# Kernel optimization log

Hardware: AMD Instinct MI355X
Metric: run time of the kernel (lower is better)

The kernel has to match this reference:

```python
import jax, jax.numpy as jnp
import numpy as np

N = 100000      # nodes
E = 1600000     # edges (avg degree 16)
D_IN, HID, D_OUT = 128, 64, 64


def setup_inputs() -> dict:
    key = jax.random.key(0)
    ks = jax.random.split(key, 32)
    rn = lambda k, shape, s=0.1: jax.random.normal(k, shape, jnp.float32) * s
    inp = {
        "x": jax.random.normal(ks[0], (N, D_IN), jnp.float32),
        "edge_index": jax.random.randint(ks[1], (2, E), 0, N, dtype=jnp.int32),
        # GAT layer 1: in=128, heads=2, C=64, concat -> 128
        "w1": rn(ks[2], (D_IN, 2 * HID)), "as1": rn(ks[3], (2, HID)),
        "ad1": rn(ks[4], (2, HID)), "b1": rn(ks[5], (2 * HID,)),
        # GAT layer 2: in=128, heads=2, C=64, concat -> 128
        "w2": rn(ks[6], (2 * HID, 2 * HID)), "as2": rn(ks[7], (2, HID)),
        "ad2": rn(ks[8], (2, HID)), "b2": rn(ks[9], (2 * HID,)),
        # GAT layer 3: in=128, heads=1, C=64, mean -> 64
        "w3": rn(ks[10], (2 * HID, D_OUT)), "as3": rn(ks[11], (1, D_OUT)),
        "ad3": rn(ks[12], (1, D_OUT)), "b3": rn(ks[13], (D_OUT,)),
        # BatchNorm (eval mode: running stats)
        "g1": 1.0 + rn(ks[14], (2 * HID,)), "be1": rn(ks[15], (2 * HID,)),
        "m1": rn(ks[16], (2 * HID,), 0.01), "v1": 1.0 + 0.1 * jax.random.uniform(ks[17], (2 * HID,)),
        "g2": 1.0 + rn(ks[18], (2 * HID,)), "be2": rn(ks[19], (2 * HID,)),
        "m2": rn(ks[20], (2 * HID,), 0.01), "v2": 1.0 + 0.1 * jax.random.uniform(ks[21], (2 * HID,)),
        "g3": 1.0 + rn(ks[22], (D_OUT,)), "be3": rn(ks[23], (D_OUT,)),
        "m3": rn(ks[24], (D_OUT,), 0.01), "v3": 1.0 + 0.1 * jax.random.uniform(ks[25], (D_OUT,)),
    }
    return inp


def _gat(h, W, a_s, a_d, b, src, dst, n, heads, concat):
    """PyG GATConv (eval, add_self_loops already applied to src/dst)."""
    C = a_s.shape[1]
    xl = (h @ W).reshape(n, heads, C)                      # [N,H,C]
    es = jnp.sum(xl * a_s, axis=-1)                        # [N,H] att_src . x
    ed = jnp.sum(xl * a_d, axis=-1)                        # [N,H]
    e = jax.nn.leaky_relu(es[src] + ed[dst], 0.2)          # [E',H]
    mx = jax.ops.segment_max(e, dst, num_segments=n)       # segment softmax over dst
    ex = jnp.exp(e - mx[dst])
    den = jax.ops.segment_sum(ex, dst, num_segments=n)
    alpha = ex / (den[dst] + 1e-16)                        # [E',H]
    out = jax.ops.segment_sum(xl[src] * alpha[:, :, None], dst, num_segments=n)
    out = out.reshape(n, heads * C) if concat else out.mean(axis=1)
    return out + b


def _bn(z, g, be, m, v):
    return (z - m) * jax.lax.rsqrt(v + 1e-5) * g + be


def reference(x, edge_index, w1, as1, ad1, b1, w2, as2, ad2, b2, w3, as3, ad3, b3,
              g1, be1, m1, v1, g2, be2, m2, v2, g3, be3, m3, v3):
    n = x.shape[0]
    loop = jnp.arange(n, dtype=edge_index.dtype)
    src = jnp.concatenate([edge_index[0], loop])           # GATConv add_self_loops=True
    dst = jnp.concatenate([edge_index[1], loop])
    z = jax.nn.relu(_bn(_gat(x, w1, as1, ad1, b1, src, dst, n, 2, True), g1, be1, m1, v1))
    z = jax.nn.relu(_bn(_gat(z, w2, as2, ad2, b2, src, dst, n, 2, True), g2, be2, m2, v2))
    z = _bn(_gat(z, w3, as3, ad3, b3, src, dst, n, 1, False), g3, be3, m3, v3)
    return z
```

## Files before the change

### kernel.cpp

```cpp
#include <hip/hip_runtime.h>
#include <hip/hip_bf16.h>
#include <cstdint>
#include <cstddef>

#define NBLK 512
#define BSH 8

typedef short bf16x8 __attribute__((ext_vector_type(8)));
typedef float f32x4 __attribute__((ext_vector_type(4)));

__device__ __forceinline__ float leaky02(float x) { return x > 0.f ? x : 0.2f * x; }
__device__ __forceinline__ float bflo(unsigned u) { return __uint_as_float(u << 16); }
__device__ __forceinline__ float bfhi(unsigned u) { return __uint_as_float(u & 0xFFFF0000u); }
__device__ __forceinline__ unsigned short f2bf(float f) {
  __hip_bfloat16 h = __float2bfloat16(f);
  return *(unsigned short*)&h;
}
__device__ __forceinline__ unsigned pack2bf(float a, float b) {
  return (unsigned)f2bf(a) | ((unsigned)f2bf(b) << 16);
}

__global__ void bucket_hist(const int* __restrict__ dst, int* __restrict__ T,
                            int E, int N, int NB, int echunk, int nchunk,
                            const float* __restrict__ w1, const float* __restrict__ w2,
                            const float* __restrict__ w3,
                            unsigned short* __restrict__ t1, unsigned short* __restrict__ t2,
                            unsigned short* __restrict__ t3) {
  int b = blockIdx.x, t = threadIdx.x;
  if (b >= NBLK) {
    int bb = b - NBLK;
    const float* W; unsigned short* Tw; int NO; int e;
    if (bb < 64)      { W = w1; Tw = t1; NO = 128; e = bb * 256 + t; }
    else if (bb < 128){ W = w2; Tw = t2; NO = 128; e = (bb - 64) * 256 + t; }
    else              { W = w3; Tw = t3; NO = 64;  e = (bb - 128) * 256 + t; }
    int c = e >> 7, k = e & 127;
    Tw[c * 128 + k] = f2bf(W[k * NO + c]);
    return;
  }
  __shared__ int hist[512];
  hist[t] = 0; hist[t + 256] = 0;
  __syncthreads();
  int e0 = b * echunk, e1 = min(E, e0 + echunk);
  for (int e = e0 + t; e < e1; e += 256) atomicAdd(&hist[dst[e] >> BSH], 1);
  int n0 = b * nchunk, n1 = min(N, n0 + nchunk);
  for (int nn = n0 + t; nn < n1; nn += 256) atomicAdd(&hist[nn >> BSH], 1);
  __syncthreads();
  for (int k = t; k < NB; k += 256) if (hist[k]) atomicAdd(&T[k], hist[k]);
}

__global__ void scan_small(const int* __restrict__ T, int* __restrict__ B,
                           int* __restrict__ C, int NB) {
  __shared__ int wsum[8];
  int t = threadIdx.x;
  int val = (t < NB) ? T[t] : 0;
  int lane = t & 63, wid = t >> 6;
  int incl = val;
  for (int off = 1; off < 64; off <<= 1) {
    int o = __shfl_up(incl, off);
    if (lane >= off) incl += o;
  }
  if (lane == 63) wsum[wid] = incl;
  __syncthreads();
  if (t == 0) { int r = 0; for (int i = 0; i < 8; ++i) { int x = wsum[i]; wsum[i] = r; r += x; } }
  __syncthreads();
  int excl = incl - val + wsum[wid];
  if (t <= NB) B[t] = excl;
  if (t < NB) C[t] = excl;
}

__global__ void bucketB2(const int* __restrict__ src, const int* __restrict__ dst,
                         int* __restrict__ C, unsigned* __restrict__ binned,
                         int E, int N, int NB, int echunk, int nchunk) {
  __shared__ int hist[512];
  __shared__ int cur[512];
  int b = blockIdx.x, t = threadIdx.x;
  hist[t] = 0; hist[t + 256] = 0;
  __syncthreads();
  int e0 = b * echunk, e1 = min(E, e0 + echunk);
  for (int e = e0 + t; e < e1; e += 256) atomicAdd(&hist[dst[e] >> BSH], 1);
  int n0 = b * nchunk, n1 = min(N, n0 + nchunk);
  for (int nn = n0 + t; nn < n1; nn += 256) atomicAdd(&hist[nn >> BSH], 1);
  __syncthreads();
  for (int k = t; k < 512; k += 256) {
    int c = hist[k];
    cur[k] = c ? atomicAdd(&C[k], c) : 0;
  }
  __syncthreads();
  for (int e = e0 + t; e < e1; e += 256) {
    int d = dst[e];
    int k = d >> BSH;
    int pos = atomicAdd(&cur[k], 1);
    binned[pos] = (unsigned)src[e] | ((unsigned)(d & 255) << 24);
  }
  for (int nn = n0 + t; nn < n1; nn += 256) {
    int k = nn >> BSH;
    int pos = atomicAdd(&cur[k], 1);
    binned[pos] = (unsigned)nn | ((unsigned)(nn & 255) << 24);
  }
}

__global__ void bucketC2(const unsigned* __restrict__ binned, const int* __restrict__ B,
                         int* __restrict__ rowp, int* __restrict__ col, int N) {
  __shared__ int cnt2[256];
  __shared__ int cur2[256];
  __shared__ int wsum[4];
  int k = blockIdx.x, t = threadIdx.x;
  int base = B[k];
  int end  = B[k + 1];
  cnt2[t] = 0;
  __syncthreads();
  for (int e = base + t; e < end; e += 256) atomicAdd(&cnt2[binned[e] >> 24], 1);
  __syncthreads();
  int v = cnt2[t];
  int incl = v;
  int lane = t & 63, wid = t >> 6;
  for (int off = 1; off < 64; off <<= 1) {
    int o = __shfl_up(incl, off);
    if (lane >= off) incl += o;
  }
  if (lane == 63) wsum[wid] = incl;
  __syncthreads();
  if (t == 0) { int r = 0; for (int i = 0; i < 4; ++i) { int x2 = wsum[i]; wsum[i] = r; r += x2; } }
  __syncthreads();
  int excl = incl - v + wsum[wid];
  int g = (k << BSH) + t;
  if (g <= N) rowp[g] = base + excl;
  cur2[t] = excl;
  __syncthreads();
  for (int e = base + t; e < end; e += 256) {
    unsigned p = binned[e];
    int pos = atomicAdd(&cur2[p >> 24], 1);
    col[base + pos] = (int)(p & 0xFFFFFFu);
  }
}

template<int NO, bool F32IN>
__launch_bounds__(256)
__global__ void gemm_mfma(const void* __restrict__ Xp,
                          const unsigned short* __restrict__ Wt,
                          unsigned short* __restrict__ Y, int n,
                          const float* __restrict__ as, const float* __restrict__ ad,
                          float* __restrict__ es, float* __restrict__ ed) {
  constexpr int NT = NO / 16;
  const int wid = threadIdx.x >> 6, lane = threadIdx.x & 63;
  const int wr0 = (blockIdx.x * 4 + wid) * 32;
  if (wr0 >= n) return;
  const int cl = lane & 15, kg = lane >> 4;

  int r0c = wr0 + cl;      if (r0c > n - 1) r0c = n - 1;
  int r1c = wr0 + 16 + cl; if (r1c > n - 1) r1c = n - 1;

  f32x4 acc[2][NT] = {};
  const unsigned short* Xb = (const unsigned short*)Xp;
  const float* Xf = (const float*)Xp;

#pragma unroll
  for (int ks = 0; ks < 4; ++ks) {
    bf16x8 a0, a1;
    if constexpr (F32IN) {
      const float* p0 = Xf + (size_t)r0c * 128 + kg * 8 + ks * 32;
      const float* p1 = Xf + (size_t)r1c * 128 + kg * 8 + ks * 32;
      float4 u0 = *(const float4*)p0, u1 = *(const float4*)(p0 + 4);
      float4 w0 = *(const float4*)p1, w1 = *(const float4*)(p1 + 4);
      a0[0] = (short)f2bf(u0.x); a0[1] = (short)f2bf(u0.y); a0[2] = (short)f2bf(u0.z); a0[3] = (short)f2bf(u0.w);
      a0[4] = (short)f2bf(u1.x); a0[5] = (short)f2bf(u1.y); a0[6] = (short)f2bf(u1.z); a0[7] = (short)f2bf(u1.w);
      a1[0] = (short)f2bf(w0.x); a1[1] = (short)f2bf(w0.y); a1[2] = (short)f2bf(w0.z); a1[3] = (short)f2bf(w0.w);
      a1[4] = (short)f2bf(w1.x); a1[5] = (short)f2bf(w1.y); a1[6] = (short)f2bf(w1.z); a1[7] = (short)f2bf(w1.w);
    } else {
      a0 = *(const bf16x8*)(Xb + (size_t)r0c * 128 + kg * 8 + ks * 32);
      a1 = *(const bf16x8*)(Xb + (size_t)r1c * 128 + kg * 8 + ks * 32);
    }
#pragma unroll
    for (int t = 0; t < NT; ++t) {
      bf16x8 bb = *(const bf16x8*)(Wt + (size_t)(cl + t * 16) * 128 + kg * 8 + ks * 32);
      acc[0][t] = __builtin_amdgcn_mfma_f32_16x16x32_bf16(a0, bb, acc[0][t], 0, 0, 0);
      acc[1][t] = __builtin_amdgcn_mfma_f32_16x16x32_bf16(a1, bb, acc[1][t], 0, 0, 0);
    }
  }

  float asv[NT], adv[NT];
#pragma unroll
  for (int t = 0; t < NT; ++t) { asv[t] = as[t * 16 + cl]; adv[t] = ad[t * 16 + cl]; }

#pragma unroll
  for (int s = 0; s < 2; ++s) {
#pragma unroll
    for (int rg = 0; rg < 4; ++rg) {
      int r = wr0 + s * 16 + kg * 4 + rg;
      float ps0 = 0.f, pd0 = 0.f, ps1 = 0.f, pd1 = 0.f;
#pragma unroll
      for (int t = 0; t < NT; ++t) {
        float a = acc[s][t][rg];
        if (NO == 128 && t >= 4) { ps1 = fmaf(a, asv[t], ps1); pd1 = fmaf(a, adv[t], pd1); }
        else                     { ps0 = fmaf(a, asv[t], ps0); pd0 = fmaf(a, adv[t], pd0); }
      }
#pragma unroll
      for (int o = 8; o; o >>= 1) {
        ps0 += __shfl_xor(ps0, o); pd0 += __shfl_xor(pd0, o);
        if (NO == 128) { ps1 += __shfl_xor(ps1, o); pd1 += __shfl_xor(pd1, o); }
      }
      if (r < n) {
        if (cl == 0) {
          if (NO == 128) {
            es[(size_t)r * 2] = ps0; es[(size_t)r * 2 + 1] = ps1;
            ed[(size_t)r * 2] = pd0; ed[(size_t)r * 2 + 1] = pd1;
          } else {
            es[r] = ps0; ed[r] = pd0;
          }
        }
#pragma unroll
        for (int t = 0; t < NT; ++t)
          Y[(size_t)r * NO + t * 16 + cl] = f2bf(acc[s][t][rg]);
      }
    }
  }
}

__launch_bounds__(256)
__global__ void aggregate2(const unsigned short* __restrict__ xl, const float* __restrict__ es,
                           const float* __restrict__ ed, const int* __restrict__ rowp,
                           const int* __restrict__ col, const float* __restrict__ bias,
                           const float* __restrict__ g, const float* __restrict__ be,
                           const float* __restrict__ m, const float* __restrict__ v,
                           uint4* __restrict__ out, int n) {
  int node = (blockIdx.x * blockDim.x + threadIdx.x) >> 6;
  int lane = threadIdx.x & 63;
  if (node >= n) return;
  const uint4* xr = (const uint4*)xl;
  int beg = rowp[node], end = rowp[node + 1];
  float2 edv = *(const float2*)&ed[(size_t)node * 2];
  const int q = lane >> 4, hl = lane & 15;

  float acc[8] = {0.f, 0.f, 0.f, 0.f, 0.f, 0.f, 0.f, 0.f};
  float dl0 = 0.f, dl1 = 0.f;

  for (int cb = beg; cb < end; cb += 64) {
    int idx = cb + lane;
    int s = 0; float w0 = 0.f, w1 = 0.f;
    if (idx < end) {
      s = col[idx];
      float2 e2 = *(const float2*)&es[(size_t)s * 2];
      w0 = __expf(leaky02(e2.x + edv.x));
      w1 = __expf(leaky02(e2.y + edv.y));
    }
    dl0 += w0; dl1 += w1;
    int cend = end - cb; if (cend > 64) cend = 64;
    int i = 0;
    for (; i + 8 <= cend; i += 8) {
      int j0 = i + q, j1 = i + 4 + q;
      int s0 = __shfl(s, j0), s1 = __shfl(s, j1);
      uint4 v0 = xr[(size_t)s0 * 16 + hl];
      uint4 v1 = xr[(size_t)s1 * 16 + hl];
      float w00 = __shfl(w0, j0), w01 = __shfl(w1, j0);
      float w10 = __shfl(w0, j1), w11 = __shfl(w1, j1);
      float W0 = (hl < 8) ? w00 : w01;
      float W1 = (hl < 8) ? w10 : w11;
      acc[0] = fmaf(W0, bflo(v0.x), acc[0]); acc[1] = fmaf(W0, bfhi(v0.x), acc[1]);
      acc[2] = fmaf(W0, bflo(v0.y), acc[2]); acc[3] = fmaf(W0, bfhi(v0.y), acc[3]);
      acc[4] = fmaf(W0, bflo(v0.z), acc[4]); acc[5] = fmaf(W0, bfhi(v0.z), acc[5]);
      acc[6] = fmaf(W0, bflo(v0.w), acc[6]); acc[7] = fmaf(W0, bfhi(v0.w), acc[7]);
      acc[0] = fmaf(W1, bflo(v1.x), acc[0]); acc[1] = fmaf(W1, bfhi(v1.x), acc[1]);
      acc[2] = fmaf(W1, bflo(v1.y), acc[2]); acc[3] = fmaf(W1, bfhi(v1.y), acc[3]);
      acc[4] = fmaf(W1, bflo(v1.z), acc[4]); acc[5] = fmaf(W1, bfhi(v1.z), acc[5]);
      acc[6] = fmaf(W1, bflo(v1.w), acc[6]); acc[7] = fmaf(W1, bfhi(v1.w), acc[7]);
    }
    for (; i < cend; i += 4) {
      int j = i + q;
      int s0 = __shfl(s, j);
      uint4 v0 = xr[(size_t)s0 * 16 + hl];
      float w00 = __shfl(w0, j), w01 = __shfl(w1, j);
      float W0 = (hl < 8) ? w00 : w01;
      acc[0] = fmaf(W0, bflo(v0.x), acc[0]); acc[1] = fmaf(W0, bfhi(v0.x), acc[1]);
      acc[2] = fmaf(W0, bflo(v0.y), acc[2]); acc[3] = fmaf(W0, bfhi(v0.y), acc[3]);
      acc[4] = fmaf(W0, bflo(v0.z), acc[4]); acc[5] = fmaf(W0, bfhi(v0.z), acc[5]);
      acc[6] = fmaf(W0, bflo(v0.w), acc[6]); acc[7] = fmaf(W0, bfhi(v0.w), acc[7]);
    }
  }

#pragma unroll
  for (int k2 = 0; k2 < 8; ++k2) {
    acc[k2] += __shfl_xor(acc[k2], 16);
    acc[k2] += __shfl_xor(acc[k2], 32);
  }
#pragma unroll
  for (int o = 32; o; o >>= 1) { dl0 += __shfl_xor(dl0, o); dl1 += __shfl_xor(dl1, o); }

  if (q == 0) {
    int c0 = hl * 8;
    float den = (hl < 8) ? dl0 : dl1;
    float inv = 1.f / (den + 1e-16f);
    float4 bi0 = *(const float4*)&bias[c0], bi1 = *(const float4*)&bias[c0 + 4];
    float4 mm0 = *(const float4*)&m[c0],    mm1 = *(const float4*)&m[c0 + 4];
    float4 vv0 = *(const float4*)&v[c0],    vv1 = *(const float4*)&v[c0 + 4];
    float4 gg0 = *(const float4*)&g[c0],    gg1 = *(const float4*)&g[c0 + 4];
    float4 bb0 = *(const float4*)&be[c0],   bb1 = *(const float4*)&be[c0 + 4];
    float r0 = (acc[0] * inv + bi0.x - mm0.x) * rsqrtf(vv0.x + 1e-5f) * gg0.x + bb0.x;
    float r1 = (acc[1] * inv + bi0.y - mm0.y) * rsqrtf(vv0.y + 1e-5f) * gg0.y + bb0.y;
    float r2 = (acc[2] * inv + bi0.z - mm0.z) * rsqrtf(vv0.z + 1e-5f) * gg0.z + bb0.z;
    float r3 = (acc[3] * inv + bi0.w - mm0.w) * rsqrtf(vv0.w + 1e-5f) * gg0.w + bb0.w;
    float r4 = (acc[4] * inv + bi1.x - mm1.x) * rsqrtf(vv1.x + 1e-5f) * gg1.x + bb1.x;
    float r5 = (acc[5] * inv + bi1.y - mm1.y) * rsqrtf(vv1.y + 1e-5f) * gg1.y + bb1.y;
    float r6 = (acc[6] * inv + bi1.z - mm1.z) * rsqrtf(vv1.z + 1e-5f) * gg1.z + bb1.z;
    float r7 = (acc[7] * inv + bi1.w - mm1.w) * rsqrtf(vv1.w + 1e-5f) * gg1.w + bb1.w;
    uint4 o;
    o.x = pack2bf(fmaxf(r0, 0.f), fmaxf(r1, 0.f));
    o.y = pack2bf(fmaxf(r2, 0.f), fmaxf(r3, 0.f));
    o.z = pack2bf(fmaxf(r4, 0.f), fmaxf(r5, 0.f));
    o.w = pack2bf(fmaxf(r6, 0.f), fmaxf(r7, 0.f));
    out[(size_t)node * 16 + hl] = o;
  }
}

__launch_bounds__(256)
__global__ void aggregate1(const unsigned short* __restrict__ xl, const float* __restrict__ es,
                           const float* __restrict__ ed, const int* __restrict__ rowp,
                           const int* __restrict__ col, const float* __restrict__ bias,
                           const float* __restrict__ g, const float* __restrict__ be,
                           const float* __restrict__ m, const float* __restrict__ v,
                           float* __restrict__ out, int n) {
  int node = (blockIdx.x * blockDim.x + threadIdx.x) >> 6;
  int lane = threadIdx.x & 63;
  if (node >= n) return;
  const uint4* xr = (const uint4*)xl;
  int beg = rowp[node], end = rowp[node + 1];
  float edv = ed[node];
  const int g8 = lane >> 3, hl = lane & 7;

  float acc[8] = {0.f, 0.f, 0.f, 0.f, 0.f, 0.f, 0.f, 0.f};
  float dl = 0.f;

  for (int cb = beg; cb < end; cb += 64) {
    int idx = cb + lane;
    int s = 0; float w = 0.f;
    if (idx < end) {
      s = col[idx];
      w = __expf(leaky02(es[s] + edv));
    }
    dl += w;
    int cend = end - cb; if (cend > 64) cend = 64;
    int i = 0;
    for (; i + 16 <= cend; i += 16) {
      int j0 = i + g8, j1 = i + 8 + g8;
      int s0 = __shfl(s, j0), s1 = __shfl(s, j1);
      uint4 v0 = xr[(size_t)s0 * 8 + hl];
      uint4 v1 = xr[(size_t)s1 * 8 + hl];
      float W0 = __shfl(w, j0), W1 = __shfl(w, j1);
      acc[0] = fmaf(W0, bflo(v0.x), acc[0]); acc[1] = fmaf(W0, bfhi(v0.x), acc[1]);
      acc[2] = fmaf(W0, bflo(v0.y), acc[2]); acc[3] = fmaf(W0, bfhi(v0.y), acc[3]);
      acc[4] = fmaf(W0, bflo(v0.z), acc[4]); acc[5] = fmaf(W0, bfhi(v0.z), acc[5]);
      acc[6] = fmaf(W0, bflo(v0.w), acc[6]); acc[7] = fmaf(W0, bfhi(v0.w), acc[7]);
      acc[0] = fmaf(W1, bflo(v1.x), acc[0]); acc[1] = fmaf(W1, bfhi(v1.x), acc[1]);
      acc[2] = fmaf(W1, bflo(v1.y), acc[2]); acc[3] = fmaf(W1, bfhi(v1.y), acc[3]);
      acc[4] = fmaf(W1, bflo(v1.z), acc[4]); acc[5] = fmaf(W1, bfhi(v1.z), acc[5]);
      acc[6] = fmaf(W1, bflo(v1.w), acc[6]); acc[7] = fmaf(W1, bfhi(v1.w), acc[7]);
    }
    for (; i < cend; i += 8) {
      int j = i + g8;
      int s0 = __shfl(s, j);
      uint4 v0 = xr[(size_t)s0 * 8 + hl];
      float W0 = __shfl(w, j);
      acc[0] = fmaf(W0, bflo(v0.x), acc[0]); acc[1] = fmaf(W0, bfhi(v0.x), acc[1]);
      acc[2] = fmaf(W0, bflo(v0.y), acc[2]); acc[3] = fmaf(W0, bfhi(v0.y), acc[3]);
      acc[4] = fmaf(W0, bflo(v0.z), acc[4]); acc[5] = fmaf(W0, bfhi(v0.z), acc[5]);
      acc[6] = fmaf(W0, bflo(v0.w), acc[6]); acc[7] = fmaf(W0, bfhi(v0.w), acc[7]);
    }
  }

#pragma unroll
  for (int k2 = 0; k2 < 8; ++k2) {
    acc[k2] += __shfl_xor(acc[k2], 8);
    acc[k2] += __shfl_xor(acc[k2], 16);
    acc[k2] += __shfl_xor(acc[k2], 32);
  }
#pragma unroll
  for (int o = 32; o; o >>= 1) dl += __shfl_xor(dl, o);

  if (lane < 8) {
    int c0 = hl * 8;
    float inv = 1.f / (dl + 1e-16f);
    float4 bi0 = *(const float4*)&bias[c0], bi1 = *(const float4*)&bias[c0 + 4];
    float4 mm0 = *(const float4*)&m[c0],    mm1 = *(const float4*)&m[c0 + 4];
    float4 vv0 = *(const float4*)&v[c0],    vv1 = *(const float4*)&v[c0 + 4];
    float4 gg0 = *(const float4*)&g[c0],    gg1 = *(const float4*)&g[c0 + 4];
    float4 bb0 = *(const float4*)&be[c0],   bb1 = *(const float4*)&be[c0 + 4];
    float4 ra, rb;
    ra.x = (acc[0] * inv + bi0.x - mm0.x) * rsqrtf(vv0.x + 1e-5f) * gg0.x + bb0.x;
    ra.y = (acc[1] * inv + bi0.y - mm0.y) * rsqrtf(vv0.y + 1e-5f) * gg0.y + bb0.y;
    ra.z = (acc[2] * inv + bi0.z - mm0.z) * rsqrtf(vv0.z + 1e-5f) * gg0.z + bb0.z;
    ra.w = (acc[3] * inv + bi0.w - mm0.w) * rsqrtf(vv0.w + 1e-5f) * gg0.w + bb0.w;
    rb.x = (acc[4] * inv + bi1.x - mm1.x) * rsqrtf(vv1.x + 1e-5f) * gg1.x + bb1.x;
    rb.y = (acc[5] * inv + bi1.y - mm1.y) * rsqrtf(vv1.y + 1e-5f) * gg1.y + bb1.y;
    rb.z = (acc[6] * inv + bi1.z - mm1.z) * rsqrtf(vv1.z + 1e-5f) * gg1.z + bb1.z;
    rb.w = (acc[7] * inv + bi1.w - mm1.w) * rsqrtf(vv1.w + 1e-5f) * gg1.w + bb1.w;
    float4* op = (float4*)(out + (size_t)node * 64 + c0);
    op[0] = ra; op[1] = rb;
  }
}

extern "C" void kernel_launch(void* const* d_in, const int* in_sizes, int n_in,
                              void* d_out, int out_size, void* d_ws, size_t ws_size,
                              hipStream_t stream) {
  const float* x   = (const float*)d_in[0];
  const int*   ei  = (const int*)d_in[1];
  const float* w1  = (const float*)d_in[2];
  const float* as1 = (const float*)d_in[3];
  const float* ad1 = (const float*)d_in[4];
  const float* b1  = (const float*)d_in[5];
  const float* w2  = (const float*)d_in[6];
  const float* as2 = (const float*)d_in[7];
  const float* ad2 = (const float*)d_in[8];
  const float* b2  = (const float*)d_in[9];
  const float* w3  = (const float*)d_in[10];
  const float* as3 = (const float*)d_in[11];
  const float* ad3 = (const float*)d_in[12];
  const float* b3  = (const float*)d_in[13];
  const float* g1  = (const float*)d_in[14];
  const float* be1 = (const float*)d_in[15];
  const float* m1  = (const float*)d_in[16];
  const float* v1  = (const float*)d_in[17];
  const float* g2  = (const float*)d_in[18];
  const float* be2 = (const float*)d_in[19];
  const float* m2  = (const float*)d_in[20];
  const float* v2  = (const float*)d_in[21];
  const float* g3  = (const float*)d_in[22];
  const float* be3 = (const float*)d_in[23];
  const float* m3  = (const float*)d_in[24];
  const float* v3  = (const float*)d_in[25];

  const int N = in_sizes[0] / 128;
  const int E = in_sizes[1] / 2;
  const int Etot = E + N;
  const int* srcp = ei;
  const int* dstp = ei + E;
  const int NB = (N + 255) >> BSH;
  const int echunk = (E + NBLK - 1) / NBLK;
  const int nchunk = (N + NBLK - 1) / NBLK;

  size_t off = 0;
  auto carve = [&](size_t bytes) {
    void* p = (char*)d_ws + off;
    off += (bytes + 255) & ~(size_t)255;
    return p;
  };
  unsigned short* Xb  = (unsigned short*)carve((size_t)N * 128 * 2);
  unsigned short* Yb  = (unsigned short*)carve((size_t)N * 128 * 2);
  float* esb  = (float*)carve((size_t)N * 2 * 4);
  float* edb  = (float*)carve((size_t)N * 2 * 4);
  int*   rowp = (int*)carve((size_t)(N + 1) * 4);
  int*   col  = (int*)carve((size_t)Etot * 4);
  unsigned* binned = (unsigned*)carve((size_t)Etot * 4);
  int* T = (int*)carve(512 * 4);
  int* B = (int*)carve(513 * 4);
  int* C = (int*)carve(512 * 4);
  unsigned short* Wt1 = (unsigned short*)carve(128 * 128 * 2);
  unsigned short* Wt2 = (unsigned short*)carve(128 * 128 * 2);
  unsigned short* Wt3 = (unsigned short*)carve(128 * 64 * 2);
  (void)ws_size; (void)n_in; (void)out_size;

  hipMemsetAsync(T, 0, NB * 4, stream);
  bucket_hist<<<NBLK + 160, 256, 0, stream>>>(dstp, T, E, N, NB, echunk, nchunk,
                                              w1, w2, w3, Wt1, Wt2, Wt3);
  scan_small<<<1, 512, 0, stream>>>(T, B, C, NB);
  bucketB2<<<NBLK, 256, 0, stream>>>(srcp, dstp, C, binned, E, N, NB, echunk, nchunk);
  bucketC2<<<NB, 256, 0, stream>>>(binned, B, rowp, col, N);

  const int gemm_grid = (N + 127) / 128;
  const int agg_grid  = (N + 3) / 4;

  gemm_mfma<128, true><<<gemm_grid, 256, 0, stream>>>(x, Wt1, Yb, N, as1, ad1, esb, edb);
  aggregate2<<<agg_grid, 256, 0, stream>>>(Yb, esb, edb, rowp, col, b1, g1, be1, m1, v1,
                                           (uint4*)Xb, N);
  gemm_mfma<128, false><<<gemm_grid, 256, 0, stream>>>(Xb, Wt2, Yb, N, as2, ad2, esb, edb);
  aggregate2<<<agg_grid, 256, 0, stream>>>(Yb, esb, edb, rowp, col, b2, g2, be2, m2, v2,
                                           (uint4*)Xb, N);
  gemm_mfma<64, false><<<gemm_grid, 256, 0, stream>>>(Xb, Wt3, Yb, N, as3, ad3, esb, edb);
  aggregate1<<<agg_grid, 256, 0, stream>>>(Yb, esb, edb, rowp, col, b3, g3, be3, m3, v3,
                                           (float*)d_out, N);
}
```

Measured before the change: 348.3 us.

## Use fixed-capacity buckets and fuse CSR sort with first GEMM

Replaces the histogram/scan/bin/sort pipeline with fixed-capacity per-bucket regions so no global prefix scan is needed, cutting the CSR build to two kernels. The per-bucket local sort runs in the same launch as the layer-1 GEMM so the two overlap, and sorts in place from an LDS copy. Aggregation kernels now read separate row begin/end arrays. The cost is a larger workspace, and any bucket exceeding the fixed capacity would be truncated.

```diff
diff --git a/kernel.cpp b/kernel.cpp
--- a/kernel.cpp
+++ b/kernel.cpp
@@ -5,6 +5,8 @@
 
 #define NBLK 512
 #define BSH 8
+#define CAPSH 13
+#define CAP (1 << CAPSH)
 
 typedef short bf16x8 __attribute__((ext_vector_type(8)));
 typedef float f32x4 __attribute__((ext_vector_type(4)));
@@ -20,130 +22,15 @@
   return (unsigned)f2bf(a) | ((unsigned)f2bf(b) << 16);
 }
 
-__global__ void bucket_hist(const int* __restrict__ dst, int* __restrict__ T,
-                            int E, int N, int NB, int echunk, int nchunk,
-                            const float* __restrict__ w1, const float* __restrict__ w2,
-                            const float* __restrict__ w3,
-                            unsigned short* __restrict__ t1, unsigned short* __restrict__ t2,
-                            unsigned short* __restrict__ t3) {
-  int b = blockIdx.x, t = threadIdx.x;
-  if (b >= NBLK) {
-    int bb = b - NBLK;
-    const float* W; unsigned short* Tw; int NO; int e;
-    if (bb < 64)      { W = w1; Tw = t1; NO = 128; e = bb * 256 + t; }
-    else if (bb < 128){ W = w2; Tw = t2; NO = 128; e = (bb - 64) * 256 + t; }
-    else              { W = w3; Tw = t3; NO = 64;  e = (bb - 128) * 256 + t; }
-    int c = e >> 7, k = e & 127;
-    Tw[c * 128 + k] = f2bf(W[k * NO + c]);
-    return;
-  }
-  __shared__ int hist[512];
-  hist[t] = 0; hist[t + 256] = 0;
-  __syncthreads();
-  int e0 = b * echunk, e1 = min(E, e0 + echunk);
-  for (int e = e0 + t; e < e1; e += 256) atomicAdd(&hist[dst[e] >> BSH], 1);
-  int n0 = b * nchunk, n1 = min(N, n0 + nchunk);
-  for (int nn = n0 + t; nn < n1; nn += 256) atomicAdd(&hist[nn >> BSH], 1);
-  __syncthreads();
-  for (int k = t; k < NB; k += 256) if (hist[k]) atomicAdd(&T[k], hist[k]);
-}
-
-__global__ void scan_small(const int* __restrict__ T, int* __restrict__ B,
-                           int* __restrict__ C, int NB) {
-  __shared__ int wsum[8];
-  int t = threadIdx.x;
-  int val = (t < NB) ? T[t] : 0;
-  int lane = t & 63, wid = t >> 6;
-  int incl = val;
-  for (int off = 1; off < 64; off <<= 1) {
-    int o = __shfl_up(incl, off);
-    if (lane >= off) incl += o;
-  }
-  if (lane == 63) wsum[wid] = incl;
-  __syncthreads();
-  if (t == 0) { int r = 0; for (int i = 0; i < 8; ++i) { int x = wsum[i]; wsum[i] = r; r += x; } }
-  __syncthreads();
-  int excl = incl - val + wsum[wid];
-  if (t <= NB) B[t] = excl;
-  if (t < NB) C[t] = excl;
-}
-
-__global__ void bucketB2(const int* __restrict__ src, const int* __restrict__ dst,
-                         int* __restrict__ C, unsigned* __restrict__ binned,
-                         int E, int N, int NB, int echunk, int nchunk) {
-  __shared__ int hist[512];
-  __shared__ int cur[512];
-  int b = blockIdx.x, t = threadIdx.x;
-  hist[t] = 0; hist[t + 256] = 0;
-  __syncthreads();
-  int e0 = b * echunk, e1 = min(E, e0 + echunk);
-  for (int e = e0 + t; e < e1; e += 256) atomicAdd(&hist[dst[e] >> BSH], 1);
-  int n0 = b * nchunk, n1 = min(N, n0 + nchunk);
-  for (int nn = n0 + t; nn < n1; nn += 256) atomicAdd(&hist[nn >> BSH], 1);
-  __syncthreads();
-  for (int k = t; k < 512; k += 256) {
-    int c = hist[k];
-    cur[k] = c ? atomicAdd(&C[k], c) : 0;
-  }
-  __syncthreads();
-  for (int e = e0 + t; e < e1; e += 256) {
-    int d = dst[e];
-    int k = d >> BSH;
-    int pos = atomicAdd(&cur[k], 1);
-    binned[pos] = (unsigned)src[e] | ((unsigned)(d & 255) << 24);
-  }
-  for (int nn = n0 + t; nn < n1; nn += 256) {
-    int k = nn >> BSH;
-    int pos = atomicAdd(&cur[k], 1);
-    binned[pos] = (unsigned)nn | ((unsigned)(nn & 255) << 24);
-  }
-}
-
-__global__ void bucketC2(const unsigned* __restrict__ binned, const int* __restrict__ B,
-                         int* __restrict__ rowp, int* __restrict__ col, int N) {
-  __shared__ int cnt2[256];
-  __shared__ int cur2[256];
-  __shared__ int wsum[4];
-  int k = blockIdx.x, t = threadIdx.x;
-  int base = B[k];
-  int end  = B[k + 1];
-  cnt2[t] = 0;
-  __syncthreads();
-  for (int e = base + t; e < end; e += 256) atomicAdd(&cnt2[binned[e] >> 24], 1);
-  __syncthreads();
-  int v = cnt2[t];
-  int incl = v;
-  int lane = t & 63, wid = t >> 6;
-  for (int off = 1; off < 64; off <<= 1) {
-    int o = __shfl_up(incl, off);
-    if (lane >= off) incl += o;
-  }
-  if (lane == 63) wsum[wid] = incl;
-  __syncthreads();
-  if (t == 0) { int r = 0; for (int i = 0; i < 4; ++i) { int x2 = wsum[i]; wsum[i] = r; r += x2; } }
-  __syncthreads();
-  int excl = incl - v + wsum[wid];
-  int g = (k << BSH) + t;
-  if (g <= N) rowp[g] = base + excl;
-  cur2[t] = excl;
-  __syncthreads();
-  for (int e = base + t; e < end; e += 256) {
-    unsigned p = binned[e];
-    int pos = atomicAdd(&cur2[p >> 24], 1);
-    col[base + pos] = (int)(p & 0xFFFFFFu);
-  }
-}
-
 template<int NO, bool F32IN>
-__launch_bounds__(256)
-__global__ void gemm_mfma(const void* __restrict__ Xp,
+__device__ void gemm_body(int bx, const void* __restrict__ Xp,
                           const unsigned short* __restrict__ Wt,
                           unsigned short* __restrict__ Y, int n,
                           const float* __restrict__ as, const float* __restrict__ ad,
                           float* __restrict__ es, float* __restrict__ ed) {
   constexpr int NT = NO / 16;
   const int wid = threadIdx.x >> 6, lane = threadIdx.x & 63;
-  const int wr0 = (blockIdx.x * 4 + wid) * 32;
+  const int wr0 = (bx * 4 + wid) * 32;
   if (wr0 >= n) return;
   const int cl = lane & 15, kg = lane >> 4;
 
@@ -217,8 +104,115 @@
 }
 
 __launch_bounds__(256)
+__global__ void mega1(const int* __restrict__ src, const int* __restrict__ dst,
+                      int* __restrict__ T, unsigned* __restrict__ binned,
+                      int E, int N, int NB, int echunk, int nchunk,
+                      const float* __restrict__ w1, const float* __restrict__ w2,
+                      const float* __restrict__ w3,
+                      unsigned short* __restrict__ t1, unsigned short* __restrict__ t2,
+                      unsigned short* __restrict__ t3) {
+  int b = blockIdx.x, t = threadIdx.x;
+  if (b >= NBLK) {
+    int bb = b - NBLK;
+    const float* W; unsigned short* Tw; int NO; int e;
+    if (bb < 64)      { W = w1; Tw = t1; NO = 128; e = bb * 256 + t; }
+    else if (bb < 128){ W = w2; Tw = t2; NO = 128; e = (bb - 64) * 256 + t; }
+    else              { W = w3; Tw = t3; NO = 64;  e = (bb - 128) * 256 + t; }
+    int c = e >> 7, k = e & 127;
+    Tw[c * 128 + k] = f2bf(W[k * NO + c]);
+    return;
+  }
+  __shared__ int hist[512];
+  __shared__ int cur[512];
+  hist[t] = 0; hist[t + 256] = 0;
+  __syncthreads();
+  int e0 = b * echunk, e1 = min(E, e0 + echunk);
+  for (int e = e0 + t; e < e1; e += 256) atomicAdd(&hist[dst[e] >> BSH], 1);
+  int n0 = b * nchunk, n1 = min(N, n0 + nchunk);
+  for (int nn = n0 + t; nn < n1; nn += 256) atomicAdd(&hist[nn >> BSH], 1);
+  __syncthreads();
+  for (int k = t; k < 512; k += 256) {
+    int c = hist[k];
+    cur[k] = c ? (k << CAPSH) + atomicAdd(&T[k], c) : 0;
+  }
+  __syncthreads();
+  for (int e = e0 + t; e < e1; e += 256) {
+    int d = dst[e];
+    int k = d >> BSH;
+    int pos = atomicAdd(&cur[k], 1);
+    binned[pos] = (unsigned)src[e] | ((unsigned)(d & 255) << 24);
+  }
+  for (int nn = n0 + t; nn < n1; nn += 256) {
+    int k = nn >> BSH;
+    int pos = atomicAdd(&cur[k], 1);
+    binned[pos] = (unsigned)nn | ((unsigned)(nn & 255) << 24);
+  }
+}
+
+__launch_bounds__(256)
+__global__ void mega2(unsigned* __restrict__ binned, const int* __restrict__ T,
+                      int* __restrict__ rowp, int* __restrict__ rowe, int N, int NB,
+                      const float* __restrict__ x, const unsigned short* __restrict__ Wt1,
+                      unsigned short* __restrict__ Y,
+                      const float* __restrict__ as1, const float* __restrict__ ad1,
+                      float* __restrict__ es, float* __restrict__ ed) {
+  int b = blockIdx.x, t = threadIdx.x;
+  if (b >= NB) {
+    gemm_body<128, true>(b - NB, x, Wt1, Y, N, as1, ad1, es, ed);
+    return;
+  }
+  __shared__ unsigned pay[CAP];
+  __shared__ int cnt2[256];
+  __shared__ int cur2[256];
+  __shared__ int wsum[4];
+  int k = b;
+  int base = k << CAPSH;
+  int cnt = T[k]; if (cnt > CAP) cnt = CAP;
+  cnt2[t] = 0;
+  __syncthreads();
+  for (int e = t; e < cnt; e += 256) {
+    unsigned p = binned[base + e];
+    pay[e] = p;
+    atomicAdd(&cnt2[p >> 24], 1);
+  }
+  __syncthreads();
+  int v = cnt2[t];
+  int incl = v;
+  int lane = t & 63, wid = t >> 6;
+  for (int off = 1; off < 64; off <<= 1) {
+    int o = __shfl_up(incl, off);
+    if (lane >= off) incl += o;
+  }
+  if (lane == 63) wsum[wid] = incl;
+  __syncthreads();
+  if (t == 0) { int r = 0; for (int i = 0; i < 4; ++i) { int x2 = wsum[i]; wsum[i] = r; r += x2; } }
+  __syncthreads();
+  int excl = incl - v + wsum[wid];
+  int g = (k << BSH) + t;
+  if (g < N) { rowp[g] = base + excl; rowe[g] = base + excl + v; }
+  cur2[t] = excl;
+  __syncthreads();
+  for (int e = t; e < cnt; e += 256) {
+    unsigned p = pay[e];
+    int pos = atomicAdd(&cur2[p >> 24], 1);
+    binned[base + pos] = p & 0xFFFFFFu;
+  }
+}
+
+template<int NO, bool F32IN>
+__launch_bounds__(256)
+__global__ void gemm_mfma(const void* __restrict__ Xp,
+                          const unsigned short* __restrict__ Wt,
+                          unsigned short* __restrict__ Y, int n,
+                          const float* __restrict__ as, const float* __restrict__ ad,
+                          float* __restrict__ es, float* __restrict__ ed) {
+  gemm_body<NO, F32IN>(blockIdx.x, Xp, Wt, Y, n, as, ad, es, ed);
+}
+
+__launch_bounds__(256)
 __global__ void aggregate2(const unsigned short* __restrict__ xl, const float* __restrict__ es,
                            const float* __restrict__ ed, const int* __restrict__ rowp,
+                           const int* __restrict__ rowe,
                            const int* __restrict__ col, const float* __restrict__ bias,
                            const float* __restrict__ g, const float* __restrict__ be,
                            const float* __restrict__ m, const float* __restrict__ v,
@@ -227,7 +221,7 @@
   int lane = threadIdx.x & 63;
   if (node >= n) return;
   const uint4* xr = (const uint4*)xl;
-  int beg = rowp[node], end = rowp[node + 1];
+  int beg = rowp[node], end = rowe[node];
   float2 edv = *(const float2*)&ed[(size_t)node * 2];
   const int q = lane >> 4, hl = lane & 15;
 
@@ -314,6 +308,7 @@
 __launch_bounds__(256)
 __global__ void aggregate1(const unsigned short* __restrict__ xl, const float* __restrict__ es,
                            const float* __restrict__ ed, const int* __restrict__ rowp,
+                           const int* __restrict__ rowe,
                            const int* __restrict__ col, const float* __restrict__ bias,
                            const float* __restrict__ g, const float* __restrict__ be,
                            const float* __restrict__ m, const float* __restrict__ v,
@@ -322,7 +317,7 @@
   int lane = threadIdx.x & 63;
   if (node >= n) return;
   const uint4* xr = (const uint4*)xl;
-  int beg = rowp[node], end = rowp[node + 1];
+  int beg = rowp[node], end = rowe[node];
   float edv = ed[node];
   const int g8 = lane >> 3, hl = lane & 7;
 
@@ -429,7 +424,6 @@
 
   const int N = in_sizes[0] / 128;
   const int E = in_sizes[1] / 2;
-  const int Etot = E + N;
   const int* srcp = ei;
   const int* dstp = ei + E;
   const int NB = (N + 255) >> BSH;
@@ -446,34 +440,31 @@
   unsigned short* Yb  = (unsigned short*)carve((size_t)N * 128 * 2);
   float* esb  = (float*)carve((size_t)N * 2 * 4);
   float* edb  = (float*)carve((size_t)N * 2 * 4);
-  int*   rowp = (int*)carve((size_t)(N + 1) * 4);
-  int*   col  = (int*)carve((size_t)Etot * 4);
-  unsigned* binned = (unsigned*)carve((size_t)Etot * 4);
+  int*   rowp = (int*)carve((size_t)N * 4);
+  int*   rowe = (int*)carve((size_t)N * 4);
+  unsigned* binned = (unsigned*)carve((size_t)NB * CAP * 4);
   int* T = (int*)carve(512 * 4);
-  int* B = (int*)carve(513 * 4);
-  int* C = (int*)carve(512 * 4);
   unsigned short* Wt1 = (unsigned short*)carve(128 * 128 * 2);
   unsigned short* Wt2 = (unsigned short*)carve(128 * 128 * 2);
   unsigned short* Wt3 = (unsigned short*)carve(128 * 64 * 2);
   (void)ws_size; (void)n_in; (void)out_size;
-
-  hipMemsetAsync(T, 0, NB * 4, stream);
-  bucket_hist<<<NBLK + 160, 256, 0, stream>>>(dstp, T, E, N, NB, echunk, nchunk,
-                                              w1, w2, w3, Wt1, Wt2, Wt3);
-  scan_small<<<1, 512, 0, stream>>>(T, B, C, NB);
-  bucketB2<<<NBLK, 256, 0, stream>>>(srcp, dstp, C, binned, E, N, NB, echunk, nchunk);
-  bucketC2<<<NB, 256, 0, stream>>>(binned, B, rowp, col, N);
+  int* col = (int*)binned;
 
   const int gemm_grid = (N + 127) / 128;
   const int agg_grid  = (N + 3) / 4;
 
-  gemm_mfma<128, true><<<gemm_grid, 256, 0, stream>>>(x, Wt1, Yb, N, as1, ad1, esb, edb);
-  aggregate2<<<agg_grid, 256, 0, stream>>>(Yb, esb, edb, rowp, col, b1, g1, be1, m1, v1,
+  hipMemsetAsync(T, 0, NB * 4, stream);
+  mega1<<<NBLK + 160, 256, 0, stream>>>(srcp, dstp, T, binned, E, N, NB, echunk, nchunk,
+                                        w1, w2, w3, Wt1, Wt2, Wt3);
+  mega2<<<NB + gemm_grid, 256, 0, stream>>>(binned, T, rowp, rowe, N, NB,
+                                            x, Wt1, Yb, as1, ad1, esb, edb);
+
+  aggregate2<<<agg_grid, 256, 0, stream>>>(Yb, esb, edb, rowp, rowe, col, b1, g1, be1, m1, v1,
                                            (uint4*)Xb, N);
   gemm_mfma<128, false><<<gemm_grid, 256, 0, stream>>>(Xb, Wt2, Yb, N, as2, ad2, esb, edb);
-  aggregate2<<<agg_grid, 256, 0, stream>>>(Yb, esb, edb, rowp, col, b2, g2, be2, m2, v2,
+  aggregate2<<<agg_grid, 256, 0, stream>>>(Yb, esb, edb, rowp, rowe, col, b2, g2, be2, m2, v2,
                                            (uint4*)Xb, N);
   gemm_mfma<64, false><<<gemm_grid, 256, 0, stream>>>(Xb, Wt3, Yb, N, as3, ad3, esb, edb);
-  aggregate1<<<agg_grid, 256, 0, stream>>>(Yb, esb, edb, rowp, col, b3, g3, be3, m3, v3,
+  aggregate1<<<agg_grid, 256, 0, stream>>>(Yb, esb, edb, rowp, rowe, col, b3, g3, be3, m3, v3,
                                            (float*)d_out, N);
 }
```

After: 324.1 us. -6.9%, faster.
